# Kernel optimization log

Measured on AMD Instinct MI355X. Metric: run time of the kernel, lower is better.

The kernel has to match this reference:

```python
import jax, jax.numpy as jnp
import numpy as np

B, T, C, H, HS = 128, 256, 384, 6, 64

def setup_inputs() -> dict:
    key = jax.random.key(0)
    k1, k2, k3, k4, k5 = jax.random.split(key, 5)
    s = 0.02
    return {
        "x": jax.random.normal(k1, (B, T, C), dtype=jnp.float32),
        "Wq": jax.random.normal(k2, (H, C, HS), dtype=jnp.float32) * s,
        "Wk": jax.random.normal(k3, (H, C, HS), dtype=jnp.float32) * s,
        "Wv": jax.random.normal(k4, (H, C, HS), dtype=jnp.float32) * s,
        "Wp": jax.random.normal(k5, (C, C), dtype=jnp.float32) * s,
        "bp": jnp.zeros((C,), dtype=jnp.float32),
    }

def reference(x, Wq, Wk, Wv, Wp, bp):
    # per-head projections: [B,H,T,HS]
    q = jnp.einsum('btc,hcd->bhtd', x, Wq)
    k = jnp.einsum('btc,hcd->bhtd', x, Wk)
    v = jnp.einsum('btc,hcd->bhtd', x, Wv)
    scale = 1.0 / jnp.sqrt(jnp.asarray(HS, dtype=x.dtype))
    # scores: [B,H,T,T], causal mask then stable softmax
    scores = jnp.einsum('bhtd,bhsd->bhts', q, k) * scale
    causal = jnp.tril(jnp.ones((T, T), dtype=bool))
    scores = jnp.where(causal, scores, -jnp.inf)
    wei = jax.nn.softmax(scores, axis=-1)
    # dropout is identity in eval mode
    out = jnp.einsum('bhts,bhsd->bhtd', wei, v)  # [B,H,T,HS]
    out = out.transpose(0, 2, 1, 3).reshape(B, T, H * HS)  # concat heads
    return out @ Wp.T + bp  # output projection
```

## Files before the change

### kernel.cpp

```cpp
#include <hip/hip_runtime.h>
#include <hip/hip_bf16.h>
#include <math.h>

#define B_   128
#define T_   256
#define C_   384
#define H_   6
#define HS_  64
#define NTOK (B_*T_)
#define NQKV (3*C_)

typedef unsigned short u16;
typedef __attribute__((ext_vector_type(8))) short bf16x8;
typedef __attribute__((ext_vector_type(4))) float f32x4;

__device__ __forceinline__ u16 f2b(float f) {
    unsigned int u = __builtin_bit_cast(unsigned int, f);
    unsigned int r = (u + 0x7FFFu + ((u >> 16) & 1u)) >> 16;
    return (u16)r;
}

__device__ __forceinline__ unsigned pk2(float a, float b) {
    unsigned r;
    asm("v_cvt_pk_bf16_f32 %0, %1, %2" : "=v"(r) : "v"(a), "v"(b));
    return r;
}

__device__ __forceinline__ float fexp2(float x) {
#if __has_builtin(__builtin_amdgcn_exp2f)
    return __builtin_amdgcn_exp2f(x);
#else
    return exp2f(x);
#endif
}

__device__ __forceinline__ void gl2lds16(const u16* g, u16* l) {
    __builtin_amdgcn_global_load_lds(
        (const __attribute__((address_space(1))) unsigned int*)g,
        (__attribute__((address_space(3))) unsigned int*)l, 16, 0, 0);
}

#define QSCALE 0.180336880f

#define J0_ (NTOK*C_/8)
#define J2_ (C_*C_/8)
#define J1_ (NQKV*C_)

__global__ __launch_bounds__(256) void prep(
    const float* __restrict__ x,  const float* __restrict__ Wq,
    const float* __restrict__ Wk, const float* __restrict__ Wv,
    const float* __restrict__ Wp,
    u16* __restrict__ xb, u16* __restrict__ wct, u16* __restrict__ wpb)
{
    int i = blockIdx.x * 256 + threadIdx.x;
    if (i < J0_) {
        const float4* s = (const float4*)x + (size_t)i * 2;
        float4 a = s[0], b = s[1];
        ushort4 o1, o2;
        o1.x = f2b(a.x); o1.y = f2b(a.y); o1.z = f2b(a.z); o1.w = f2b(a.w);
        o2.x = f2b(b.x); o2.y = f2b(b.y); o2.z = f2b(b.z); o2.w = f2b(b.w);
        ((ushort4*)xb)[(size_t)i * 2]     = o1;
        ((ushort4*)xb)[(size_t)i * 2 + 1] = o2;
    } else if (i < J0_ + J2_) {
        int j = i - J0_;
        const float4* s = (const float4*)Wp + (size_t)j * 2;
        float4 a = s[0], b = s[1];
        ushort4 o1, o2;
        o1.x = f2b(a.x); o1.y = f2b(a.y); o1.z = f2b(a.z); o1.w = f2b(a.w);
        o2.x = f2b(b.x); o2.y = f2b(b.y); o2.z = f2b(b.z); o2.w = f2b(b.w);
        ((ushort4*)wpb)[(size_t)j * 2]     = o1;
        ((ushort4*)wpb)[(size_t)j * 2 + 1] = o2;
    } else {
        int j = i - J0_ - J2_;
        if (j < J1_) {
            int n = j / C_, c = j % C_;
            int h = n / 192, rem = n % 192;
            int p = rem >> 6, d = rem & 63;
            const float* W = (p == 0 ? Wq : (p == 1 ? Wk : Wv));
            wct[j] = f2b(W[(h * C_ + c) * HS_ + d]);
        }
    }
}

__global__ __launch_bounds__(512, 2) void qkv_attn(
    const u16* __restrict__ xb, const u16* __restrict__ wct,
    u16* __restrict__ yb)
{
    __shared__ __align__(16) u16 SM[65536];
    u16* A0 = SM;
    u16* A1 = SM + 16384;
    u16* B0 = SM + 32768;
    u16* B1 = SM + 45056;
    u16* Qs = SM;
    u16* Vs = SM + 16384;
    u16* Ks = SM + 32768;
    u16* Pr = SM + 57344;

    const int gid = blockIdx.x;
    const int lin = (gid & 7) * 96 + (gid >> 3);
    const int b = lin / 6, h = lin % 6;

    const int tid = threadIdx.x;
    const int w = tid >> 6, lane = tid & 63;
    const int lm = lane & 15, qd = lane >> 4;
    const int wm = (w >> 1) * 64, wn = (w & 1) * 96;

    const int schunk = (lane & 7) ^ ((lane >> 3) & 7);
    const u16* gA0 = xb  + (size_t)(b * T_ + w * 32 + (lane >> 3)) * C_ + schunk * 8;
    const u16* gB0 = wct + (size_t)(h * 192 + w * 24 + (lane >> 3)) * C_ + schunk * 8;
    u16* lA[2] = { A0 + (w * 32) * 64, A1 + (w * 32) * 64 };
    u16* lB[2] = { B0 + (w * 24) * 64, B1 + (w * 24) * 64 };

    f32x4 acc[4][6];
    #pragma unroll
    for (int mi = 0; mi < 4; ++mi)
        #pragma unroll
        for (int ni = 0; ni < 6; ++ni)
            acc[mi][ni] = (f32x4){0.f, 0.f, 0.f, 0.f};

    #pragma unroll
    for (int s = 0; s < 2; ++s) {
        #pragma unroll
        for (int j = 0; j < 4; ++j)
            gl2lds16(gA0 + s * 64 + j * 8 * C_, lA[s] + j * 8 * 64);
        #pragma unroll
        for (int j = 0; j < 3; ++j)
            gl2lds16(gB0 + s * 64 + j * 8 * C_, lB[s] + j * 8 * 64);
    }

    #pragma unroll
    for (int k0i = 0; k0i < 6; ++k0i) {
        if (k0i < 5) asm volatile("s_waitcnt vmcnt(7)" ::: "memory");
        else         asm volatile("s_waitcnt vmcnt(0)" ::: "memory");
        __builtin_amdgcn_s_barrier();
        const u16* Ab = (k0i & 1) ? A1 : A0;
        const u16* Bb = (k0i & 1) ? B1 : B0;

        #pragma unroll
        for (int ks = 0; ks < 2; ++ks) {
            bf16x8 af[4], bfr[6];
            #pragma unroll
            for (int mi = 0; mi < 4; ++mi) {
                const int row = wm + mi * 16 + lm;
                const int sl = (ks * 4 + qd) ^ (lm & 7);
                af[mi] = *(const bf16x8*)&Ab[row * 64 + sl * 8];
            }
            #pragma unroll
            for (int ni = 0; ni < 6; ++ni) {
                const int row = wn + ni * 16 + lm;
                const int sl = (ks * 4 + qd) ^ (lm & 7);
                bfr[ni] = *(const bf16x8*)&Bb[row * 64 + sl * 8];
            }
            #pragma unroll
            for (int mi = 0; mi < 4; ++mi)
                #pragma unroll
                for (int ni = 0; ni < 6; ++ni)
                    acc[mi][ni] = __builtin_amdgcn_mfma_f32_16x16x32_bf16(
                        af[mi], bfr[ni], acc[mi][ni], 0, 0, 0);
        }
        asm volatile("" ::: "memory");
        __builtin_amdgcn_s_barrier();
        if (k0i < 4) {
            #pragma unroll
            for (int j = 0; j < 4; ++j)
                gl2lds16(gA0 + (k0i + 2) * 64 + j * 8 * C_, lA[k0i & 1] + j * 8 * 64);
            #pragma unroll
            for (int j = 0; j < 3; ++j)
                gl2lds16(gB0 + (k0i + 2) * 64 + j * 8 * C_, lB[k0i & 1] + j * 8 * 64);
        }
    }

    __syncthreads();
    const int wnu = __builtin_amdgcn_readfirstlane(wn);
    #pragma unroll
    for (int mi = 0; mi < 4; ++mi) {
        const int t0 = wm + mi * 16 + qd * 4;
        #pragma unroll
        for (int ni = 0; ni < 6; ++ni) {
            const int cat = wnu + ni * 16;
            const int n = wn + ni * 16 + lm;
            if (cat < 64) {
                unsigned p0 = pk2(acc[mi][ni][0] * QSCALE, acc[mi][ni][1] * QSCALE);
                unsigned p1 = pk2(acc[mi][ni][2] * QSCALE, acc[mi][ni][3] * QSCALE);
                #pragma unroll
                for (int r = 0; r < 4; ++r) {
                    const int t = t0 + r;
                    const unsigned pv = (r < 2) ? p0 : p1;
                    Qs[t * 64 + (((n >> 3) ^ (t & 7)) << 3) + (n & 7)]
                        = (r & 1) ? (u16)(pv >> 16) : (u16)pv;
                }
            } else if (cat < 128) {
                const int d = n - 64;
                unsigned p0 = pk2(acc[mi][ni][0], acc[mi][ni][1]);
                unsigned p1 = pk2(acc[mi][ni][2], acc[mi][ni][3]);
                #pragma unroll
                for (int r = 0; r < 4; ++r) {
                    const int t = t0 + r;
                    const unsigned pv = (r < 2) ? p0 : p1;
                    Ks[t * 64 + (((d >> 3) ^ (t & 7)) << 3) + (d & 7)]
                        = (r & 1) ? (u16)(pv >> 16) : (u16)pv;
                }
            } else {
                const int d = n - 128;
                const int ch = t0 >> 3;
                const int pos = (ch & 16) | ((ch ^ (d & 15)) & 15);
                unsigned p0 = pk2(acc[mi][ni][0], acc[mi][ni][1]);
                unsigned p1 = pk2(acc[mi][ni][2], acc[mi][ni][3]);
                unsigned* dst = (unsigned*)&Vs[d * 256 + pos * 8 + (t0 & 7)];
                dst[0] = p0; dst[1] = p1;
            }
        }
    }
    __syncthreads();

    const int trg0 = w * 16;
    const int trg1 = 128 + (7 - w) * 16;
    bf16x8 aq[2][2];
    #pragma unroll
    for (int rg = 0; rg < 2; ++rg) {
        const int t = (rg ? trg1 : trg0) + lm;
        #pragma unroll
        for (int ks = 0; ks < 2; ++ks)
            aq[rg][ks] = *(const bf16x8*)
                &Qs[t * 64 + (((ks * 4 + qd) ^ (t & 7)) << 3)];
    }

    f32x4 oacc[2][4];
    float ms[2][4], ls[2][4];
    #pragma unroll
    for (int rg = 0; rg < 2; ++rg) {
        #pragma unroll
        for (int ni = 0; ni < 4; ++ni) oacc[rg][ni] = (f32x4){0.f, 0.f, 0.f, 0.f};
        #pragma unroll
        for (int r = 0; r < 4; ++r) { ms[rg][r] = -INFINITY; ls[rg][r] = 0.f; }
    }

    u16* Pw = Pr + w * 1024;

#define QKT16(ST, AQ, J0V)                                                    \
    do {                                                                      \
        _Pragma("unroll")                                                     \
        for (int ni_ = 0; ni_ < 4; ++ni_) ST[ni_] = (f32x4){0.f,0.f,0.f,0.f}; \
        _Pragma("unroll")                                                     \
        for (int ks_ = 0; ks_ < 2; ++ks_) {                                   \
            _Pragma("unroll")                                                 \
            for (int ni_ = 0; ni_ < 4; ++ni_) {                               \
                const int krow_ = (J0V) + ni_ * 16 + lm;                      \
                const int sl_ = (ks_ * 4 + qd) ^ (lm & 7);                    \
                bf16x8 bk_ = *(const bf16x8*)&Ks[krow_ * 64 + sl_ * 8];       \
                ST[ni_] = __builtin_amdgcn_mfma_f32_16x16x32_bf16(            \
                    AQ[ks_], bk_, ST[ni_], 0, 0, 0);                          \
            }                                                                 \
        }                                                                     \
    } while (0)

    #pragma unroll
    for (int rg = 0; rg < 2; ++rg) {
        const int trg = rg ? trg1 : trg0;
        const int kmax = trg >> 6;

        f32x4 stc[4];
        QKT16(stc, aq[rg], 0);

        for (int kt = 0; kt <= kmax; ++kt) {
            const int j0 = kt * 64;
            const bool needmask = (kt == kmax);

            f32x4 stn[4];
            if (kt < kmax)
                QKT16(stn, aq[rg], j0 + 64);

            float vals[4][4], rowmax[4];
            #pragma unroll
            for (int r = 0; r < 4; ++r) rowmax[r] = -INFINITY;
            #pragma unroll
            for (int ni = 0; ni < 4; ++ni) {
                const int s_g = j0 + ni * 16 + lm;
                #pragma unroll
                for (int r = 0; r < 4; ++r) {
                    float sc = stc[ni][r];
                    if (needmask) {
                        const int t_g = trg + qd * 4 + r;
                        sc = (s_g > t_g) ? -1e30f : sc;
                    }
                    vals[ni][r] = sc;
                    rowmax[r] = fmaxf(rowmax[r], sc);
                }
            }
            #pragma unroll
            for (int msk = 1; msk <= 8; msk <<= 1)
                #pragma unroll
                for (int r = 0; r < 4; ++r)
                    rowmax[r] = fmaxf(rowmax[r], __shfl_xor(rowmax[r], msk, 64));

            float corr[4], rowsum[4];
            #pragma unroll
            for (int r = 0; r < 4; ++r) {
                const float mn = fmaxf(ms[rg][r], rowmax[r]);
                corr[r] = fexp2(ms[rg][r] - mn);
                ms[rg][r] = mn;
                rowsum[r] = 0.f;
            }
            #pragma unroll
            for (int ni = 0; ni < 4; ++ni) {
                float pv[4];
                #pragma unroll
                for (int r = 0; r < 4; ++r) {
                    pv[r] = fexp2(vals[ni][r] - ms[rg][r]);
                    rowsum[r] += pv[r];
                }
                const int pcol = ni * 16 + lm;
                unsigned p01 = pk2(pv[0], pv[1]);
                unsigned p23 = pk2(pv[2], pv[3]);
                #pragma unroll
                for (int r = 0; r < 4; ++r) {
                    const int prow = qd * 4 + r;
                    const unsigned pp = (r < 2) ? p01 : p23;
                    Pw[prow * 64 + (((pcol >> 3) ^ (prow & 7)) << 3) + (pcol & 7)]
                        = (r & 1) ? (u16)(pp >> 16) : (u16)pp;
                }
            }
            #pragma unroll
            for (int msk = 1; msk <= 8; msk <<= 1)
                #pragma unroll
                for (int r = 0; r < 4; ++r)
                    rowsum[r] += __shfl_xor(rowsum[r], msk, 64);
            #pragma unroll
            for (int r = 0; r < 4; ++r) ls[rg][r] = ls[rg][r] * corr[r] + rowsum[r];
            #pragma unroll
            for (int ni = 0; ni < 4; ++ni)
                #pragma unroll
                for (int r = 0; r < 4; ++r)
                    oacc[rg][ni][r] *= corr[r];

            #pragma unroll
            for (int ks = 0; ks < 2; ++ks) {
                const int rch = (ks * 4 + qd) ^ (lm & 7);
                bf16x8 pa = *(const bf16x8*)&Pw[lm * 64 + rch * 8];
                #pragma unroll
                for (int ni = 0; ni < 4; ++ni) {
                    const int d = ni * 16 + lm;
                    const int cj = kt * 8 + ks * 4 + qd;
                    const int pos = (cj & 16) | ((cj ^ (d & 15)) & 15);
                    bf16x8 bv = *(const bf16x8*)&Vs[d * 256 + pos * 8];
                    oacc[rg][ni] = __builtin_amdgcn_mfma_f32_16x16x32_bf16(
                        pa, bv, oacc[rg][ni], 0, 0, 0);
                }
            }

            if (kt < kmax) {
                #pragma unroll
                for (int ni = 0; ni < 4; ++ni) stc[ni] = stn[ni];
            }
        }
    }

    __syncthreads();
    u16 (*yt)[72] = (u16(*)[72])SM;
    #pragma unroll
    for (int rg = 0; rg < 2; ++rg) {
        const int trow = (rg ? trg1 : trg0) + qd * 4;
        float inv[4];
        #pragma unroll
        for (int r = 0; r < 4; ++r) inv[r] = __builtin_amdgcn_rcpf(ls[rg][r]);
        #pragma unroll
        for (int ni = 0; ni < 4; ++ni) {
            unsigned p01 = pk2(oacc[rg][ni][0] * inv[0], oacc[rg][ni][1] * inv[1]);
            unsigned p23 = pk2(oacc[rg][ni][2] * inv[2], oacc[rg][ni][3] * inv[3]);
            #pragma unroll
            for (int r = 0; r < 4; ++r) {
                const unsigned pp = (r < 2) ? p01 : p23;
                yt[trow + r][ni * 16 + lm] = (r & 1) ? (u16)(pp >> 16) : (u16)pp;
            }
        }
    }
    __syncthreads();
    #pragma unroll
    for (int rr = 0; rr < 4; ++rr) {
        const int row = rr * 64 + (tid >> 3);
        const int col = (tid & 7) * 8;
        bf16x8 vv = *(const bf16x8*)&yt[row][col];
        *(bf16x8*)(yb + ((size_t)(b * T_ + row)) * C_ + h * 64 + col) = vv;
    }
}

__global__ __launch_bounds__(512, 4) void gemm_proj(
    const u16* __restrict__ yb, const u16* __restrict__ wpb,
    const float* __restrict__ bp, float* __restrict__ out)
{
    __shared__ __align__(16) u16 SMEM[256 * 64 + 128 * 64];
    u16* As = SMEM;
    u16* Bs = SMEM + 256 * 64;

    const int gid  = blockIdx.x;
    const int xcd  = gid & 7;
    const int j_   = gid >> 3;
    const int colb = j_ % 3;
    const int rowb = (j_ / 3) * 8 + xcd;
    const int m0g  = rowb * 256;
    const int n0g  = colb * 128;

    const int tid = threadIdx.x;
    const int w = tid >> 6, lane = tid & 63;
    const int lm = lane & 15, qd = lane >> 4;
    const int wm = (w >> 1) * 64, wn = (w & 1) * 64;

    const int schunk = (lane & 7) ^ ((lane >> 3) & 7);
    const u16* gA = yb  + (size_t)(m0g + w * 32 + (lane >> 3)) * C_ + schunk * 8;
    const u16* gB = wpb + (size_t)(n0g + w * 16 + (lane >> 3)) * C_ + schunk * 8;
    u16* lA = &As[(w * 32) * 64];
    u16* lB = &Bs[(w * 16) * 64];

    f32x4 acc[4][4];
    #pragma unroll
    for (int mi = 0; mi < 4; ++mi)
        #pragma unroll
        for (int ni = 0; ni < 4; ++ni)
            acc[mi][ni] = (f32x4){0.f, 0.f, 0.f, 0.f};

    for (int k0 = 0; k0 < C_; k0 += 64) {
        __syncthreads();
        #pragma unroll
        for (int j = 0; j < 4; ++j)
            gl2lds16(gA + j * 8 * C_, lA + j * 8 * 64);
        #pragma unroll
        for (int j = 0; j < 2; ++j)
            gl2lds16(gB + j * 8 * C_, lB + j * 8 * 64);
        gA += 64; gB += 64;
        __syncthreads();

        #pragma unroll
        for (int ks = 0; ks < 2; ++ks) {
            bf16x8 af[4], bfr[4];
            #pragma unroll
            for (int mi = 0; mi < 4; ++mi) {
                const int row = wm + mi * 16 + lm;
                const int sl = (ks * 4 + qd) ^ (lm & 7);
                af[mi] = *(const bf16x8*)&As[row * 64 + sl * 8];
            }
            #pragma unroll
            for (int ni = 0; ni < 4; ++ni) {
                const int row = wn + ni * 16 + lm;
                const int sl = (ks * 4 + qd) ^ (lm & 7);
                bfr[ni] = *(const bf16x8*)&Bs[row * 64 + sl * 8];
            }
            #pragma unroll
            for (int mi = 0; mi < 4; ++mi)
                #pragma unroll
                for (int ni = 0; ni < 4; ++ni)
                    acc[mi][ni] = __builtin_amdgcn_mfma_f32_16x16x32_bf16(
                        af[mi], bfr[ni], acc[mi][ni], 0, 0, 0);
        }
    }

    float bpv[4];
    #pragma unroll
    for (int ni = 0; ni < 4; ++ni) bpv[ni] = bp[n0g + wn + ni * 16 + lm];

    float (*tb)[132] = (float(*)[132])SMEM;
    const int rloc = tid >> 3;
    #pragma unroll
    for (int mi = 0; mi < 4; ++mi) {
        __syncthreads();
        #pragma unroll
        for (int ni = 0; ni < 4; ++ni)
            #pragma unroll
            for (int r = 0; r < 4; ++r)
                tb[(w >> 1) * 16 + qd * 4 + r][wn + ni * 16 + lm]
                    = acc[mi][ni][r] + bpv[ni];
        __syncthreads();
        const int m = m0g + (rloc >> 4) * 64 + mi * 16 + (rloc & 15);
        #pragma unroll
        for (int jj = 0; jj < 4; ++jj) {
            const int cc = (tid & 7) * 4 + jj * 32;
            float4 vv = *(const float4*)&tb[rloc][cc];
            *(float4*)(out + (size_t)m * C_ + n0g + cc) = vv;
        }
    }
}

extern "C" void kernel_launch(void* const* d_in, const int* in_sizes, int n_in,
                              void* d_out, int out_size, void* d_ws, size_t ws_size,
                              hipStream_t stream)
{
    const float* x  = (const float*)d_in[0];
    const float* Wq = (const float*)d_in[1];
    const float* Wk = (const float*)d_in[2];
    const float* Wv = (const float*)d_in[3];
    const float* Wp = (const float*)d_in[4];
    const float* bp = (const float*)d_in[5];
    float* out = (float*)d_out;

    u16* xb  = (u16*)d_ws;
    u16* wct = xb  + (size_t)NTOK * C_;
    u16* wpb = wct + (size_t)NQKV * C_;
    u16* yb  = wpb + (size_t)C_ * C_;

    const int prep_blocks = (J0_ + J2_ + J1_ + 255) / 256;
    hipLaunchKernelGGL(prep, dim3(prep_blocks), dim3(256), 0, stream,
                       x, Wq, Wk, Wv, Wp, xb, wct, wpb);

    hipLaunchKernelGGL(qkv_attn, dim3(B_ * H_), dim3(512), 0, stream,
                       xb, wct, yb);

    hipLaunchKernelGGL(gemm_proj, dim3((NTOK / 256) * (C_ / 128)), dim3(512), 0, stream,
                       yb, wpb, bp, out);
}
```

Before: 181.0 us.

## Double-buffer output projection GEMM and widen tiles to 256x192

The output-projection GEMM now uses 256x192 tiles, so the grid is exactly 256 blocks, one per CU. It double-buffers the K-loop, with async global-to-LDS loads for the next slices overlapping the current MFMA work. Explicit vmcnt waits and raw barriers replace the full __syncthreads pairs. In exchange it uses more LDS and accumulator registers per block, lowers occupancy to 2 blocks per CU, and needs the vmcnt counts to match the number of loads issued.

```diff
diff --git a/kernel.cpp b/kernel.cpp
--- a/kernel.cpp
+++ b/kernel.cpp
@@ -384,86 +384,102 @@
     }
 }
 
-__global__ __launch_bounds__(512, 4) void gemm_proj(
+__global__ __launch_bounds__(512, 2) void gemm_proj(
     const u16* __restrict__ yb, const u16* __restrict__ wpb,
     const float* __restrict__ bp, float* __restrict__ out)
 {
-    __shared__ __align__(16) u16 SMEM[256 * 64 + 128 * 64];
-    u16* As = SMEM;
-    u16* Bs = SMEM + 256 * 64;
-
-    const int gid  = blockIdx.x;
-    const int xcd  = gid & 7;
-    const int j_   = gid >> 3;
-    const int colb = j_ % 3;
-    const int rowb = (j_ / 3) * 8 + xcd;
-    const int m0g  = rowb * 256;
-    const int n0g  = colb * 128;
+    __shared__ __align__(16) u16 SMEM[57344];
+    u16* A0 = SMEM;
+    u16* A1 = SMEM + 16384;
+    u16* B0 = SMEM + 32768;
+    u16* B1 = SMEM + 45056;
+
+    const int gid = blockIdx.x;
+    const int lin = (gid & 7) * 32 + (gid >> 3);
+    const int rowb = lin >> 1, colb = lin & 1;
+    const int m0g = rowb * 256, n0g = colb * 192;
 
     const int tid = threadIdx.x;
     const int w = tid >> 6, lane = tid & 63;
     const int lm = lane & 15, qd = lane >> 4;
-    const int wm = (w >> 1) * 64, wn = (w & 1) * 64;
+    const int wm = (w >> 1) * 64, wn = (w & 1) * 96;
 
     const int schunk = (lane & 7) ^ ((lane >> 3) & 7);
     const u16* gA = yb  + (size_t)(m0g + w * 32 + (lane >> 3)) * C_ + schunk * 8;
-    const u16* gB = wpb + (size_t)(n0g + w * 16 + (lane >> 3)) * C_ + schunk * 8;
-    u16* lA = &As[(w * 32) * 64];
-    u16* lB = &Bs[(w * 16) * 64];
-
-    f32x4 acc[4][4];
+    const u16* gB = wpb + (size_t)(n0g + w * 24 + (lane >> 3)) * C_ + schunk * 8;
+    u16* lA[2] = { A0 + (w * 32) * 64, A1 + (w * 32) * 64 };
+    u16* lB[2] = { B0 + (w * 24) * 64, B1 + (w * 24) * 64 };
+
+    f32x4 acc[4][6];
     #pragma unroll
     for (int mi = 0; mi < 4; ++mi)
         #pragma unroll
-        for (int ni = 0; ni < 4; ++ni)
+        for (int ni = 0; ni < 6; ++ni)
             acc[mi][ni] = (f32x4){0.f, 0.f, 0.f, 0.f};
 
-    for (int k0 = 0; k0 < C_; k0 += 64) {
-        __syncthreads();
+    #pragma unroll
+    for (int s = 0; s < 2; ++s) {
         #pragma unroll
         for (int j = 0; j < 4; ++j)
-            gl2lds16(gA + j * 8 * C_, lA + j * 8 * 64);
-        #pragma unroll
-        for (int j = 0; j < 2; ++j)
-            gl2lds16(gB + j * 8 * C_, lB + j * 8 * 64);
-        gA += 64; gB += 64;
-        __syncthreads();
+            gl2lds16(gA + s * 64 + j * 8 * C_, lA[s] + j * 8 * 64);
+        #pragma unroll
+        for (int j = 0; j < 3; ++j)
+            gl2lds16(gB + s * 64 + j * 8 * C_, lB[s] + j * 8 * 64);
+    }
+
+    #pragma unroll
+    for (int k0i = 0; k0i < 6; ++k0i) {
+        if (k0i < 5) asm volatile("s_waitcnt vmcnt(7)" ::: "memory");
+        else         asm volatile("s_waitcnt vmcnt(0)" ::: "memory");
+        __builtin_amdgcn_s_barrier();
+        const u16* Ab = (k0i & 1) ? A1 : A0;
+        const u16* Bb = (k0i & 1) ? B1 : B0;
 
         #pragma unroll
         for (int ks = 0; ks < 2; ++ks) {
-            bf16x8 af[4], bfr[4];
+            bf16x8 af[4], bfr[6];
             #pragma unroll
             for (int mi = 0; mi < 4; ++mi) {
                 const int row = wm + mi * 16 + lm;
                 const int sl = (ks * 4 + qd) ^ (lm & 7);
-                af[mi] = *(const bf16x8*)&As[row * 64 + sl * 8];
-            }
-            #pragma unroll
-            for (int ni = 0; ni < 4; ++ni) {
+                af[mi] = *(const bf16x8*)&Ab[row * 64 + sl * 8];
+            }
+            #pragma unroll
+            for (int ni = 0; ni < 6; ++ni) {
                 const int row = wn + ni * 16 + lm;
                 const int sl = (ks * 4 + qd) ^ (lm & 7);
-                bfr[ni] = *(const bf16x8*)&Bs[row * 64 + sl * 8];
+                bfr[ni] = *(const bf16x8*)&Bb[row * 64 + sl * 8];
             }
             #pragma unroll
             for (int mi = 0; mi < 4; ++mi)
                 #pragma unroll
-                for (int ni = 0; ni < 4; ++ni)
+                for (int ni = 0; ni < 6; ++ni)
                     acc[mi][ni] = __builtin_amdgcn_mfma_f32_16x16x32_bf16(
                         af[mi], bfr[ni], acc[mi][ni], 0, 0, 0);
         }
-    }
-
-    float bpv[4];
-    #pragma unroll
-    for (int ni = 0; ni < 4; ++ni) bpv[ni] = bp[n0g + wn + ni * 16 + lm];
-
-    float (*tb)[132] = (float(*)[132])SMEM;
+        asm volatile("" ::: "memory");
+        __builtin_amdgcn_s_barrier();
+        if (k0i < 4) {
+            #pragma unroll
+            for (int j = 0; j < 4; ++j)
+                gl2lds16(gA + (k0i + 2) * 64 + j * 8 * C_, lA[k0i & 1] + j * 8 * 64);
+            #pragma unroll
+            for (int j = 0; j < 3; ++j)
+                gl2lds16(gB + (k0i + 2) * 64 + j * 8 * C_, lB[k0i & 1] + j * 8 * 64);
+        }
+    }
+
+    float bpv[6];
+    #pragma unroll
+    for (int ni = 0; ni < 6; ++ni) bpv[ni] = bp[n0g + wn + ni * 16 + lm];
+
+    float (*tb)[196] = (float(*)[196])SMEM;
     const int rloc = tid >> 3;
     #pragma unroll
     for (int mi = 0; mi < 4; ++mi) {
         __syncthreads();
         #pragma unroll
-        for (int ni = 0; ni < 4; ++ni)
+        for (int ni = 0; ni < 6; ++ni)
             #pragma unroll
             for (int r = 0; r < 4; ++r)
                 tb[(w >> 1) * 16 + qd * 4 + r][wn + ni * 16 + lm]
@@ -471,7 +487,7 @@
         __syncthreads();
         const int m = m0g + (rloc >> 4) * 64 + mi * 16 + (rloc & 15);
         #pragma unroll
-        for (int jj = 0; jj < 4; ++jj) {
+        for (int jj = 0; jj < 6; ++jj) {
             const int cc = (tid & 7) * 4 + jj * 32;
             float4 vv = *(const float4*)&tb[rloc][cc];
             *(float4*)(out + (size_t)m * C_ + n0g + cc) = vv;
@@ -503,6 +519,6 @@
     hipLaunchKernelGGL(qkv_attn, dim3(B_ * H_), dim3(512), 0, stream,
                        xb, wct, yb);
 
-    hipLaunchKernelGGL(gemm_proj, dim3((NTOK / 256) * (C_ / 128)), dim3(512), 0, stream,
+    hipLaunchKernelGGL(gemm_proj, dim3(256), dim3(512), 0, stream,
                        yb, wpb, bp, out);
 }
```

Result: no change. 183.4 us (+1.3%).
